# Kernel optimization log

Measured on AMD Instinct MI355X. Metric: run time of the kernel, lower is better.

## Reference

```python
import jax, jax.numpy as jnp
import numpy as np

B, S, W = 64, 512, 16
E, TE, CE, CC = 300, 50, 50, 50
HID, TGT = 256, 16
VOCAB, TAGV, CHARV = 5002, 50, 100
IN = E + TE + CC  # 400


def setup_inputs() -> dict:
    key = jax.random.key(0)
    ks = jax.random.split(key, 24)
    sc = 0.1
    embed_table = (jax.random.normal(ks[0], (VOCAB, E)) * sc).at[0].set(0.0)
    tag_table = (jax.random.normal(ks[1], (TAGV, TE)) * sc).at[0].set(0.0)
    char_table = (jax.random.normal(ks[2], (CHARV, CE)) * sc).at[0].set(0.0)
    return {
        "X": jax.random.randint(ks[3], (B, S), 0, VOCAB),
        "labels_m": jax.random.uniform(ks[4], (B, S)),
        "tags": jax.random.randint(ks[5], (B, S), 0, TAGV),
        "chars": jax.random.randint(ks[6], (B, S, W), 0, CHARV),
        "embed_table": embed_table,
        "tag_table": tag_table,
        "char_table": char_table,
        "conv_w": jax.random.normal(ks[7], (CC, CE, 3)) * sc,
        "conv_b": jax.random.normal(ks[8], (CC,)) * sc,
        "w_ih_f": jax.random.normal(ks[9], (4 * HID, IN)) * sc,
        "w_hh_f": jax.random.normal(ks[10], (4 * HID, HID)) * sc,
        "b_ih_f": jax.random.normal(ks[11], (4 * HID,)) * sc,
        "b_hh_f": jax.random.normal(ks[12], (4 * HID,)) * sc,
        "w_ih_b": jax.random.normal(ks[13], (4 * HID, IN)) * sc,
        "w_hh_b": jax.random.normal(ks[14], (4 * HID, HID)) * sc,
        "b_ih_b": jax.random.normal(ks[15], (4 * HID,)) * sc,
        "b_hh_b": jax.random.normal(ks[16], (4 * HID,)) * sc,
        "fc_w": jax.random.normal(ks[17], (TGT, 2 * HID)) * sc,
        "fc_b": jax.random.normal(ks[18], (TGT,)) * sc,
        "A": jax.random.normal(ks[19], (TGT, TGT)),
        "wd": jax.random.normal(ks[20], (2 * HID,)),
    }


def _lstm_dir(xs, w_ih, w_hh, b_ih, b_hh, reverse):
    # xs: [S, B, IN] ; PyTorch gate order i,f,g,o
    h0 = jnp.zeros((xs.shape[1], w_hh.shape[1]), xs.dtype)

    def step(carry, x):
        h, c = carry
        g = x @ w_ih.T + h @ w_hh.T + (b_ih + b_hh)
        i, f, gg, o = jnp.split(g, 4, axis=-1)
        c = jax.nn.sigmoid(f) * c + jax.nn.sigmoid(i) * jnp.tanh(gg)
        h = jax.nn.sigmoid(o) * jnp.tanh(c)
        return (h, c), h

    _, hs = jax.lax.scan(step, (h0, h0), xs, reverse=reverse)
    return hs


def _features(X, labels_m, tags, chars, embed_table, tag_table, char_table,
              conv_w, conv_b, w_ih_f, w_hh_f, b_ih_f, b_hh_f,
              w_ih_b, w_hh_b, b_ih_b, b_hh_b, fc_w, fc_b, wd):
    embed = embed_table[X]          # [B,S,E]
    tag_embed = tag_table[tags]     # [B,S,TE]
    ce = char_table[chars]          # [B,S,W,CE]
    ce = ce.transpose(0, 3, 1, 2).reshape(B, CE, S * W)  # [B,CE,S*W]
    conv = jax.lax.conv_general_dilated(
        ce, conv_w, window_strides=(1,), padding=((1, 1),),
        dimension_numbers=("NCH", "OIH", "NCH")) + conv_b[None, :, None]
    char_conv = conv.reshape(B, CC, S, W).max(axis=3).transpose(0, 2, 1)  # [B,S,CC]
    feat = jnp.concatenate([embed, tag_embed, char_conv], axis=2)  # [B,S,IN]
    xs = feat.transpose(1, 0, 2)  # [S,B,IN]
    hf = _lstm_dir(xs, w_ih_f, w_hh_f, b_ih_f, b_hh_f, reverse=False)
    hb = _lstm_dir(xs, w_ih_b, w_hh_b, b_ih_b, b_hh_b, reverse=True)
    H = jnp.concatenate([hf, hb], axis=-1).transpose(1, 0, 2)  # [B,S,2H]
    H = H + labels_m[:, :, None] * wd[None, None, :]
    return H @ fc_w.T + fc_b  # [B,S,TGT]


def _viterbi(P, A):
    Xs = P.transpose(1, 0, 2)  # [S,B,T]
    b_idx = jnp.arange(P.shape[0])

    def vstep(delta, x):
        scores = delta[:, :, None] + A[None] + x[:, None, :]  # [B,prev,cur]
        return scores.max(axis=1), (scores.max(axis=1), scores.argmax(axis=1))

    deltaL, (drest, psis) = jax.lax.scan(vstep, Xs[0], Xs[1:])
    deltas = jnp.concatenate([Xs[0][None], drest], axis=0)  # [S,B,T]
    psi_end = deltaL.argmax(axis=1)                          # [B]
    score0 = deltaL[b_idx, psi_end]

    def back(carry, inp):
        tag, sc = carry
        psi_t, delta_t = inp
        prev = psi_t[b_idx, tag]
        return (prev, sc + delta_t[b_idx, prev]), prev

    (_, score), prevs = jax.lax.scan(back, (psi_end, score0),
                                     (psis, deltas[:-1]), reverse=True)
    path = jnp.concatenate([prevs, psi_end[None]], axis=0).T  # [B,S]
    return path, score


def reference(X, labels_m, tags, chars, embed_table, tag_table, char_table,
              conv_w, conv_b, w_ih_f, w_hh_f, b_ih_f, b_hh_f,
              w_ih_b, w_hh_b, b_ih_b, b_hh_b, fc_w, fc_b, A, wd):
    P = _features(X, labels_m, tags, chars, embed_table, tag_table, char_table,
                  conv_w, conv_b, w_ih_f, w_hh_f, b_ih_f, b_hh_f,
                  w_ih_b, w_hh_b, b_ih_b, b_hh_b, fc_w, fc_b, wd)
    return _viterbi(P, A)
```

## Files before the change

kernel.cpp:

```cpp
#include <hip/hip_runtime.h>


#define DEV __device__ __forceinline__
typedef unsigned short u16;
typedef unsigned int   u32;
typedef unsigned char  u8;
typedef signed char    s8;
using short8  = __attribute__((ext_vector_type(8))) short;
using f32x4   = __attribute__((ext_vector_type(4))) float;
using int4v   = __attribute__((ext_vector_type(4))) int;

DEV float bf2f(u16 u){ union{u32 i; float f;} v; v.i = ((u32)u)<<16; return v.f; }
DEV u16 f2bf(float f){ u32 x = __float_as_uint(f); return (u16)((x + 0x7fffu + ((x>>16)&1u)) >> 16); }
DEV float sigf(float x){ return __builtin_amdgcn_rcpf(1.f + __expf(-x)); }
DEV float tanh_f(float x){ return 1.f - 2.f*__builtin_amdgcn_rcpf(__expf(2.f*x) + 1.f); }

typedef __attribute__((address_space(1))) const u32 GU;
typedef __attribute__((address_space(3))) u32 LU;
DEV void gld_lds16(const void* g, void* l){
  __builtin_amdgcn_global_load_lds((GU*)g, (LU*)l, 16, 0, 0);
}
DEV void bar_l(){
  __builtin_amdgcn_sched_barrier(0);
  asm volatile("s_waitcnt lgkmcnt(0)" ::: "memory");
  __builtin_amdgcn_s_barrier();
  __builtin_amdgcn_sched_barrier(0);
}

static const size_t OFF_GI   = 0;
static const size_t OFF_P    = 0;
static const size_t OFF_DL   = OFF_P  + (size_t)32768*16*4;
static const size_t OFF_PSI  = OFF_DL + (size_t)32768*16*4;
static const size_t OFF_B    = (size_t)134217728;
static const size_t OFF_WIH  = OFF_B    + (size_t)33554432;
static const size_t OFF_WQ   = OFF_WIH  + (size_t)1703936;
static const size_t OFF_SC   = OFF_WQ   + (size_t)524288;
static const size_t OFF_BIAS = OFF_SC   + 8192;
static const size_t OFF_WFC  = OFF_BIAS + 8192;
static const size_t REQUIRED = OFF_WFC  + 256;

__global__ void k0_pack(const float* __restrict__ wihf, const float* __restrict__ wihb,
                        u16* __restrict__ wih)
{
  int n = blockIdx.x, tid = threadIdx.x;
  const float* src = (n < 1024) ? (wihf + (size_t)n*400) : (wihb + (size_t)(n-1024)*400);
  u32* dst = (u32*)(wih + (size_t)n*416);
  if (tid < 208){
    int j = tid*2;
    u32 v = 0u;
    if (j < 400){
      float2 f = *(const float2*)(src + j);
      v = (u32)f2bf(f.x) | ((u32)f2bf(f.y) << 16);
    }
    dst[tid] = v;
  }
}

__global__ __launch_bounds__(256) void k0qm(
    const float* __restrict__ whhf, const float* __restrict__ whhb,
    s8* __restrict__ wq, float* __restrict__ sc2,
    const float* bihf, const float* bhhf, const float* bihb, const float* bhhb,
    const float* fcw, const float* wdp, float* bias, float* wfc)
{
  __shared__ float red[256];
  const int tid = threadIdx.x;
  if (blockIdx.x == 512){
    for (int n = tid; n < 2048; n += 256){
      bias[n] = (n < 1024) ? (bihf[n] + bhhf[n]) : (bihb[n-1024] + bhhb[n-1024]);
    }
    const int cur = tid & 15, part = tid >> 4;
    float s = 0.f;
    for (int k = part*32; k < part*32 + 32; k++) s += fcw[cur*512 + k] * wdp[k];
    red[tid] = s;
    __syncthreads();
    if (tid < 16){
      float t = 0.f;
      #pragma unroll
      for (int p = 0; p < 16; p++) t += red[p*16 + tid];
      wfc[tid] = t;
    }
    return;
  }
  const int row = blockIdx.x*4 + (tid >> 6);
  const int lane = tid & 63;
  const float* src = (row < 1024) ? (whhf + (size_t)row*256)
                                  : (whhb + (size_t)(row-1024)*256);
  f32x4 v = *(const f32x4*)(src + lane*4);
  float m = fmaxf(fmaxf(fabsf(v[0]), fabsf(v[1])), fmaxf(fabsf(v[2]), fabsf(v[3])));
  #pragma unroll
  for (int d = 1; d < 64; d <<= 1) m = fmaxf(m, __shfl_xor(m, d, 64));
  float inv = 127.f / (m + 1e-30f);
  u32 pack = 0;
  #pragma unroll
  for (int e = 0; e < 4; e++){
    int q = (int)rintf(v[e]*inv);
    q = q > 127 ? 127 : (q < -127 ? -127 : q);
    pack |= ((u32)(u8)(s8)q) << (8*e);
  }
  const int dir = row >> 10, n = row & 1023;
  const int g = n >> 8, j = n & 255, w2 = j >> 4, lr2 = j & 15;
  const int kk = lane >> 4, lq2 = (lane >> 2) & 3, e4 = lane & 3;
  u32* wq32 = (u32*)wq;
  wq32[dir*65536 + (((g*16 + w2)*4 + kk)*64 + lq2*16 + lr2)*4 + e4] = pack;
  if (lane == 0) sc2[row] = m * (1.f/16129.f);
}

__global__ __launch_bounds__(256) void k1_feat(
    const int* __restrict__ X, const int* __restrict__ tg, const int* __restrict__ ch,
    const float* __restrict__ etab, const float* __restrict__ ttab, const float* __restrict__ ctab,
    const float* __restrict__ cw, const float* __restrict__ cb, u16* __restrict__ feat)
{
  const int b = blockIdx.y, tid = threadIdx.x;
  __shared__ float ce_s[66*60];
  __shared__ float w_s[150*52];
  for (int i = tid; i < 7500; i += 256){
    int cc = i/150, r2 = i - cc*150;
    int ce = r2/3, dc = r2 - ce*3;
    w_s[(cc*3 + dc)*52 + ce] = cw[i];
  }
  const int li = tid & 15, jg = tid >> 4;

  for (int it = 0; it < 8; it++){
    const int sb = blockIdx.x*8 + it;
    __syncthreads();
    for (int i = tid; i < 600; i += 256){
      int wl = i/150, j = i - wl*150;
      int s = sb*4 + wl;
      int idx = X[b*512 + s];
      float2 f = *(const float2*)(etab + (size_t)idx*300 + j*2);
      *(u32*)(feat + (size_t)(s*64 + b)*416 + j*2) = (u32)f2bf(f.x) | ((u32)f2bf(f.y) << 16);
    }
    for (int i = tid; i < 100; i += 256){
      int wl = i/25, j = i - wl*25;
      int s = sb*4 + wl;
      int idx = tg[b*512 + s];
      float2 f = *(const float2*)(ttab + (size_t)idx*50 + j*2);
      *(u32*)(feat + (size_t)(s*64 + b)*416 + 300 + j*2) = (u32)f2bf(f.x) | ((u32)f2bf(f.y) << 16);
    }
    if (tid < 32){
      int wl = tid>>3, j = tid&7;
      int s = sb*4 + wl;
      *(u32*)(feat + (size_t)(s*64 + b)*416 + 400 + j*2) = 0u;
    }
    for (int i = tid; i < 3300; i += 256){
      int qq = i/50, ce = i - qq*50;
      int p = sb*64 - 1 + qq;
      float v = 0.f;
      if (p >= 0 && p < 8192){
        int ci = ch[b*8192 + p];
        v = ctab[ci*50 + ce];
      }
      ce_s[qq*60 + ce] = v;
    }
    __syncthreads();
    float acc[4][3];
    #pragma unroll
    for (int k=0;k<4;k++){ acc[k][0]=0.f; acc[k][1]=0.f; acc[k][2]=0.f; }
    #pragma unroll
    for (int dc = 0; dc < 3; dc++){
      for (int ceb = 0; ceb < 48; ceb += 4){
        f32x4 w0 = *(const f32x4*)&w_s[((3*jg+0)*3 + dc)*52 + ceb];
        f32x4 w1 = *(const f32x4*)&w_s[((3*jg+1)*3 + dc)*52 + ceb];
        f32x4 w2 = *(const f32x4*)&w_s[((3*jg+2)*3 + dc)*52 + ceb];
        #pragma unroll
        for (int k = 0; k < 4; k++){
          f32x4 cv = *(const f32x4*)&ce_s[(16*k + li + dc)*60 + ceb];
          #pragma unroll
          for (int e = 0; e < 4; e++){
            acc[k][0] += cv[e]*w0[e];
            acc[k][1] += cv[e]*w1[e];
            acc[k][2] += cv[e]*w2[e];
          }
        }
      }
      float w0a = w_s[((3*jg+0)*3+dc)*52 + 48], w0b = w_s[((3*jg+0)*3+dc)*52 + 49];
      float w1a = w_s[((3*jg+1)*3+dc)*52 + 48], w1b = w_s[((3*jg+1)*3+dc)*52 + 49];
      float w2a = w_s[((3*jg+2)*3+dc)*52 + 48], w2b = w_s[((3*jg+2)*3+dc)*52 + 49];
      #pragma unroll
      for (int k = 0; k < 4; k++){
        float ca = ce_s[(16*k + li + dc)*60 + 48];
        float cb2 = ce_s[(16*k + li + dc)*60 + 49];
        acc[k][0] += ca*w0a + cb2*w0b;
        acc[k][1] += ca*w1a + cb2*w1b;
        acc[k][2] += ca*w2a + cb2*w2b;
      }
    }
    #pragma unroll
    for (int m = 1; m < 16; m <<= 1)
      #pragma unroll
      for (int k=0;k<4;k++)
        #pragma unroll
        for (int c=0;c<3;c++)
          acc[k][c] = fmaxf(acc[k][c], __shfl_xor(acc[k][c], m, 64));
    if (li == 0){
      #pragma unroll
      for (int k=0;k<4;k++)
        #pragma unroll
        for (int c=0;c<3;c++){
          int cc = 3*jg + c;
          int s = sb*4 + k;
          feat[(size_t)(s*64 + b)*416 + 350 + cc] = f2bf(acc[k][c] + cb[cc]);
        }
    }
    if (tid < 128){
      int pl = tid & 63, cc = 48 + (tid >> 6);
      float a2 = 0.f;
      #pragma unroll
      for (int dc = 0; dc < 3; dc++){
        for (int ceb = 0; ceb < 48; ceb += 4){
          f32x4 wv = *(const f32x4*)&w_s[(cc*3 + dc)*52 + ceb];
          f32x4 cv = *(const f32x4*)&ce_s[(pl + dc)*60 + ceb];
          a2 += cv[0]*wv[0] + cv[1]*wv[1] + cv[2]*wv[2] + cv[3]*wv[3];
        }
        a2 += ce_s[(pl+dc)*60 + 48]*w_s[(cc*3+dc)*52 + 48]
            + ce_s[(pl+dc)*60 + 49]*w_s[(cc*3+dc)*52 + 49];
      }
      #pragma unroll
      for (int m = 1; m < 16; m <<= 1) a2 = fmaxf(a2, __shfl_xor(a2, m, 64));
      if ((tid & 15) == 0){
        int s = sb*4 + ((tid & 63) >> 4);
        feat[(size_t)(s*64 + b)*416 + 350 + cc] = f2bf(a2 + cb[cc]);
      }
    }
  }
}

__global__ __launch_bounds__(256) void k2_gemm(
    const u16* __restrict__ featp, const u16* __restrict__ wihp,
    const float* __restrict__ bias, u16* __restrict__ gi)
{
  const int m0 = blockIdx.y*128, n0 = blockIdx.x*128;
  const int tid = threadIdx.x, wv = tid>>6, lane = tid&63;
  const int lr = lane & 15, lq = lane >> 4;
  const int wm = (wv>>1)*64, wn = (wv&1)*64;
  __shared__ u16 As[4096], Bs[4096];
  f32x4 acc[4][4];
  #pragma unroll
  for (int a=0;a<4;a++)
    #pragma unroll
    for (int c=0;c<4;c++) acc[a][c] = (f32x4){0.f,0.f,0.f,0.f};
  for (int k0 = 0; k0 < 416; k0 += 32){
    __syncthreads();
    #pragma unroll
    for (int i = 0; i < 2; i++){
      int c = i*4 + wv;
      gld_lds16(featp + (size_t)(m0 + c*16 + (lane>>2))*416 + k0 + (lane&3)*8, &As[c*512]);
      gld_lds16(wihp  + (size_t)(n0 + c*16 + (lane>>2))*416 + k0 + (lane&3)*8, &Bs[c*512]);
    }
    __syncthreads();
    short8 af[4], bfr[4];
    #pragma unroll
    for (int mt=0; mt<4; mt++) af[mt]  = *(const short8*)(As + (wm + mt*16 + lr)*32 + lq*8);
    #pragma unroll
    for (int nt=0; nt<4; nt++) bfr[nt] = *(const short8*)(Bs + (wn + nt*16 + lr)*32 + lq*8);
    #pragma unroll
    for (int mt=0; mt<4; mt++)
      #pragma unroll
      for (int nt=0; nt<4; nt++)
        acc[mt][nt] = __builtin_amdgcn_mfma_f32_16x16x32_bf16(af[mt], bfr[nt], acc[mt][nt], 0,0,0);
  }
  #pragma unroll
  for (int nt=0; nt<4; nt++){
    float bv = bias[n0 + wn + nt*16 + lr];
    #pragma unroll
    for (int mt=0; mt<4; mt++)
      #pragma unroll
      for (int r=0; r<4; r++)
        gi[(size_t)(m0 + wm + mt*16 + lq*4 + r)*2048 + n0 + wn + nt*16 + lr]
            = f2bf(acc[mt][nt][r] + bv);
  }
}

__global__ __launch_bounds__(512, 2) void k3_lstm(
    const s8* __restrict__ wq, const float* __restrict__ sc2,
    const u16* __restrict__ gi, u16* __restrict__ hcat)
{
  const int dir = blockIdx.x >> 5;
  const int bb  = (blockIdx.x & 31) * 2;
  const int tid = threadIdx.x;
  const int w = tid >> 6, lane = tid & 63;
  const int lr = lane & 15, lq = lane >> 4;
  const int cb = tid >> 8, cj = tid & 255;

  __shared__ s8 Hs[2][4096];
  __shared__ float xbuf[2048];

  const s8* wqd = wq + dir*262144;
  int4v bq[2][4][4];
  #pragma unroll
  for (int sl = 0; sl < 2; sl++)
    #pragma unroll
    for (int g = 0; g < 4; g++)
      #pragma unroll
      for (int kk = 0; kk < 4; kk++)
        bq[sl][g][kk] = *(const int4v*)(wqd + (((((g*16 + 2*w + sl)*4 + kk)*64) + lane) << 4));

  float scl[4];
  #pragma unroll
  for (int g = 0; g < 4; g++) scl[g] = sc2[dir*1024 + g*256 + cj];

  *(uint2*)&Hs[0][tid*8] = (uint2){0u,0u};
  *(uint2*)&Hs[1][tid*8] = (uint2){0u,0u};

  float cst = 0.f;
  const ptrdiff_t dstep = dir ? -(ptrdiff_t)131072 : (ptrdiff_t)131072;
  const u16* g0 = gi + (size_t)((dir ? 511 : 0)*64 + bb + cb)*2048 + dir*1024 + cj;
  u32 gcur[4], gn1[4], gn2[4];
  #pragma unroll
  for (int g = 0; g < 4; g++) gcur[g] = g0[g*256];
  const u16* g1 = g0 + dstep;
  #pragma unroll
  for (int g = 0; g < 4; g++) gn1[g] = g1[g*256];
  const u16* gpref = g1;
  __syncthreads();

  #pragma unroll 1
  for (int t = 0; t < 512; t++){
    const int s = dir ? (511 - t) : t;
    if (t + 2 < 512) gpref += dstep;
    #pragma unroll
    for (int g = 0; g < 4; g++) gn2[g] = gpref[g*256];
    const s8* hb = Hs[t & 1];
    int4v aq[4];
    #pragma unroll
    for (int kk = 0; kk < 4; kk++)
      aq[kk] = *(const int4v*)(hb + lr*256 + ((kk*64 + lq*16) ^ (lr << 4)));
    int4v acc[2][4];
    #pragma unroll
    for (int sl = 0; sl < 2; sl++)
      #pragma unroll
      for (int g = 0; g < 4; g++) acc[sl][g] = (int4v){0,0,0,0};
    #pragma unroll
    for (int kk = 0; kk < 4; kk++)
      #pragma unroll
      for (int sl = 0; sl < 2; sl++)
        #pragma unroll
        for (int g = 0; g < 4; g++)
          acc[sl][g] = __builtin_amdgcn_mfma_i32_16x16x64_i8(aq[kk], bq[sl][g][kk], acc[sl][g], 0,0,0);
    if (lq == 0){
      #pragma unroll
      for (int sl = 0; sl < 2; sl++){
        const int j = (2*w + sl)*16 + lr;
        #pragma unroll
        for (int r = 0; r < 2; r++){
          f32x4 v = (f32x4){(float)acc[sl][0][r], (float)acc[sl][1][r],
                            (float)acc[sl][2][r], (float)acc[sl][3][r]};
          *(f32x4*)&xbuf[(r*256 + j)*4] = v;
        }
      }
    }
    bar_l();
    f32x4 p = *(const f32x4*)&xbuf[tid*4];
    float g4[4];
    #pragma unroll
    for (int g = 0; g < 4; g++) g4[g] = bf2f((u16)gcur[g]) + p[g]*scl[g];
    float iv = sigf(g4[0]), fv = sigf(g4[1]);
    float gg = tanh_f(g4[2]), ov = sigf(g4[3]);
    float c = fv*cst + iv*gg;
    cst = c;
    float h = ov * tanh_f(c);
    hcat[(size_t)(s*64 + bb + cb)*512 + dir*256 + cj] = f2bf(h);
    Hs[(t + 1) & 1][cb*256 + (cj ^ (cb << 4))] = (s8)(int)rintf(h * 127.f);
    #pragma unroll
    for (int g = 0; g < 4; g++){ gcur[g] = gn1[g]; gn1[g] = gn2[g]; }
    bar_l();
  }
}

__global__ __launch_bounds__(256) void k4_fc(
    const u16* __restrict__ hcat, const float* __restrict__ fcw, const float* __restrict__ fcb,
    const float* __restrict__ lmp, const float* __restrict__ wfc, float* __restrict__ Pout)
{
  const int wv = threadIdx.x >> 6, lane = threadIdx.x & 63;
  const int lr = lane & 15, lq = lane >> 4;
  const int mt = blockIdx.x*4 + wv;
  short8 bfr[16];
  #pragma unroll
  for (int kk = 0; kk < 16; kk++){
    const float* wr = fcw + (size_t)lr*512 + kk*32 + lq*8;
    f32x4 w0 = *(const f32x4*)wr;
    f32x4 w1 = *(const f32x4*)(wr + 4);
    short8 sv;
    #pragma unroll
    for (int e = 0; e < 4; e++){ sv[e] = (short)f2bf(w0[e]); sv[4+e] = (short)f2bf(w1[e]); }
    bfr[kk] = sv;
  }
  f32x4 acc = (f32x4){0.f,0.f,0.f,0.f};
  #pragma unroll
  for (int kk = 0; kk < 16; kk++){
    short8 af = *(const short8*)(hcat + (size_t)(mt*16 + lr)*512 + kk*32 + lq*8);
    acc = __builtin_amdgcn_mfma_f32_16x16x32_bf16(af, bfr[kk], acc, 0,0,0);
  }
  const int cur = lr;
  float fb = fcb[cur];
  float wf = wfc[cur];
  #pragma unroll
  for (int r = 0; r < 4; r++){
    int m = mt*16 + lq*4 + r;
    int b = m & 63, s = m >> 6;
    float lmv = lmp[b*512 + s];
    Pout[(size_t)m*16 + cur] = acc[r] + fb + lmv*wf;
  }
}

__global__ __launch_bounds__(64) void k5_vit(
    const float* __restrict__ Pg, const float* __restrict__ Am,
    float* __restrict__ dout, float* __restrict__ dl, u8* __restrict__ psi)
{
  const int b = blockIdx.x, lane = threadIdx.x;
  const int cur = lane >> 2, q = lane & 3;
  float Ar[4];
  #pragma unroll
  for (int r = 0; r < 4; r++) Ar[r] = Am[(4*q + r)*16 + cur];
  float val = Pg[(size_t)b*16 + cur];
  if (q == 0) dl[(size_t)b*16 + cur] = val;

#define FSTEP(X, S) { \
    float best = -3.0e38f; int bi = 0; \
    _Pragma("unroll") \
    for (int r = 0; r < 4; r++){ \
      float dp = __shfl(val, (4*q + r)*4, 64); \
      float sc = (dp + Ar[r]) + (X); \
      if (sc > best){ best = sc; bi = 4*q + r; } \
    } \
    { float ov = __shfl_xor(best, 1, 64); int oi = __shfl_xor(bi, 1, 64); \
      if (ov > best || (ov == best && oi < bi)){ best = ov; bi = oi; } } \
    { float ov = __shfl_xor(best, 2, 64); int oi = __shfl_xor(bi, 2, 64); \
      if (ov > best || (ov == best && oi < bi)){ best = ov; bi = oi; } } \
    val = best; \
    if (q == 0){ \
      dl[(size_t)((S)*64 + b)*16 + cur] = best; \
      psi[(size_t)((S)*64 + b)*16 + cur] = (u8)bi; \
    } }

  float x0 = Pg[(size_t)(1*64 + b)*16 + cur];
  float x1 = Pg[(size_t)(2*64 + b)*16 + cur];
  float x2 = Pg[(size_t)(3*64 + b)*16 + cur];
  float x3 = Pg[(size_t)(4*64 + b)*16 + cur];
  for (int s = 1; s < 512; s += 4){
    FSTEP(x0, s);
    if (s + 4 < 512) x0 = Pg[(size_t)((s+4)*64 + b)*16 + cur];
    if (s + 1 < 512) FSTEP(x1, s+1);
    if (s + 5 < 512) x1 = Pg[(size_t)((s+5)*64 + b)*16 + cur];
    if (s + 2 < 512) FSTEP(x2, s+2);
    if (s + 6 < 512) x2 = Pg[(size_t)((s+6)*64 + b)*16 + cur];
    if (s + 3 < 512) FSTEP(x3, s+3);
    if (s + 7 < 512) x3 = Pg[(size_t)((s+7)*64 + b)*16 + cur];
  }
#undef FSTEP

  float bv = val; int bix = cur;
  #pragma unroll
  for (int m = 1; m < 64; m <<= 1){
    float ov = __shfl_xor(bv, m, 64);
    int   oi = __shfl_xor(bix, m, 64);
    if (ov > bv || (ov == bv && oi < bix)){ bv = ov; bix = oi; }
  }
  int tag = bix;
  float score = bv;
  if (lane == 0) dout[b*512 + 511] = (float)tag;

#define BSTEP(PV, DV, T) { \
    int prev = __shfl((PV), tag, 64); \
    score += __shfl((DV), prev, 64); \
    if (lane == 0) dout[b*512 + (T)] = (float)prev; \
    tag = prev; }

  int   p0 = 0, p1 = 0, p2 = 0, p3 = 0;
  float d0 = 0.f, d1 = 0.f, d2 = 0.f, d3 = 0.f;
  if (lane < 16){
    p0 = psi[(size_t)(511*64 + b)*16 + lane]; d0 = dl[(size_t)(510*64 + b)*16 + lane];
    p1 = psi[(size_t)(510*64 + b)*16 + lane]; d1 = dl[(size_t)(509*64 + b)*16 + lane];
    p2 = psi[(size_t)(509*64 + b)*16 + lane]; d2 = dl[(size_t)(508*64 + b)*16 + lane];
    p3 = psi[(size_t)(508*64 + b)*16 + lane]; d3 = dl[(size_t)(507*64 + b)*16 + lane];
  }
  for (int t = 510; t >= 0; t -= 4){
    BSTEP(p0, d0, t);
    if (t - 4 >= 0 && lane < 16){
      p0 = psi[(size_t)((t-3)*64 + b)*16 + lane]; d0 = dl[(size_t)((t-4)*64 + b)*16 + lane];
    }
    if (t - 1 >= 0) BSTEP(p1, d1, t-1);
    if (t - 5 >= 0 && lane < 16){
      p1 = psi[(size_t)((t-4)*64 + b)*16 + lane]; d1 = dl[(size_t)((t-5)*64 + b)*16 + lane];
    }
    if (t - 2 >= 0) BSTEP(p2, d2, t-2);
    if (t - 6 >= 0 && lane < 16){
      p2 = psi[(size_t)((t-5)*64 + b)*16 + lane]; d2 = dl[(size_t)((t-6)*64 + b)*16 + lane];
    }
    if (t - 3 >= 0) BSTEP(p3, d3, t-3);
    if (t - 7 >= 0 && lane < 16){
      p3 = psi[(size_t)((t-6)*64 + b)*16 + lane]; d3 = dl[(size_t)((t-7)*64 + b)*16 + lane];
    }
  }
#undef BSTEP
  if (lane == 0) dout[32768 + b] = score;
}

extern "C" void kernel_launch(void* const* d_in, const int* in_sizes, int n_in,
                              void* d_out, int out_size, void* d_ws, size_t ws_size,
                              hipStream_t stream)
{
  (void)in_sizes; (void)n_in; (void)out_size;
  if (ws_size < REQUIRED) return;

  const int*   X    = (const int*)d_in[0];
  const float* lm   = (const float*)d_in[1];
  const int*   tg   = (const int*)d_in[2];
  const int*   ch   = (const int*)d_in[3];
  const float* etab = (const float*)d_in[4];
  const float* ttab = (const float*)d_in[5];
  const float* ctab = (const float*)d_in[6];
  const float* cw   = (const float*)d_in[7];
  const float* cb   = (const float*)d_in[8];
  const float* wihf = (const float*)d_in[9];
  const float* whhf = (const float*)d_in[10];
  const float* bihf = (const float*)d_in[11];
  const float* bhhf = (const float*)d_in[12];
  const float* wihb = (const float*)d_in[13];
  const float* whhb = (const float*)d_in[14];
  const float* bihb = (const float*)d_in[15];
  const float* bhhb = (const float*)d_in[16];
  const float* fcw  = (const float*)d_in[17];
  const float* fcb  = (const float*)d_in[18];
  const float* Am   = (const float*)d_in[19];
  const float* wdp  = (const float*)d_in[20];

  char* ws = (char*)d_ws;
  u16*   gi   = (u16*)(ws + OFF_GI);
  u16*   feat = (u16*)(ws + OFF_B);
  u16*   hcat = (u16*)(ws + OFF_B);
  u16*   wih  = (u16*)(ws + OFF_WIH);
  s8*    wq   = (s8*)(ws + OFF_WQ);
  float* sc2  = (float*)(ws + OFF_SC);
  float* Pg   = (float*)(ws + OFF_P);
  float* dlt  = (float*)(ws + OFF_DL);
  u8*    psi  = (u8*)(ws + OFF_PSI);
  float* bias = (float*)(ws + OFF_BIAS);
  float* wfc  = (float*)(ws + OFF_WFC);
  float* dout = (float*)d_out;

  k0_pack<<<2048, 256, 0, stream>>>(wihf, wihb, wih);
  k0qm<<<513, 256, 0, stream>>>(whhf, whhb, wq, sc2,
                                bihf, bhhf, bihb, bhhb, fcw, wdp, bias, wfc);
  k1_feat<<<dim3(16, 64), 256, 0, stream>>>(X, tg, ch, etab, ttab, ctab, cw, cb, feat);
  k2_gemm<<<dim3(16, 256), 256, 0, stream>>>(feat, wih, bias, gi);
  k3_lstm<<<64, 512, 0, stream>>>(wq, sc2, gi, hcat);
  k4_fc<<<512, 256, 0, stream>>>(hcat, fcw, fcb, lm, wfc, Pg);
  k5_vit<<<64, 64, 0, stream>>>(Pg, Am, dout, dlt, psi);
}
```

Before: 1.194 ms.

## Merge weight-prep kernels, raise MFMA priority, rework Viterbi with readlane broadcasts

Merges the two weight-preparation kernels into a single launch to save one kernel launch. Raises wave priority around the int8 MFMA block in the LSTM recurrence. Rewrites the Viterbi forward step so each lane computes a full 16-way max tree from scalar-broadcast deltas (readlane) instead of cross-lane shuffles, and uses readlane in backtracking. This trades shuffle latency on the serial critical path for more per-lane ALU work and scalar broadcasts. The argmax tie-break order in the tree may differ from the previous code.

```diff
diff --git a/kernel.cpp b/kernel.cpp
--- a/kernel.cpp
+++ b/kernel.cpp
@@ -14,6 +14,9 @@
 DEV u16 f2bf(float f){ u32 x = __float_as_uint(f); return (u16)((x + 0x7fffu + ((x>>16)&1u)) >> 16); }
 DEV float sigf(float x){ return __builtin_amdgcn_rcpf(1.f + __expf(-x)); }
 DEV float tanh_f(float x){ return 1.f - 2.f*__builtin_amdgcn_rcpf(__expf(2.f*x) + 1.f); }
+DEV float rdlane_f(float v, int l){
+  return __uint_as_float(__builtin_amdgcn_readlane(__float_as_uint(v), l));
+}
 
 typedef __attribute__((address_space(1))) const u32 GU;
 typedef __attribute__((address_space(3))) u32 LU;
@@ -39,32 +42,32 @@
 static const size_t OFF_WFC  = OFF_BIAS + 8192;
 static const size_t REQUIRED = OFF_WFC  + 256;
 
-__global__ void k0_pack(const float* __restrict__ wihf, const float* __restrict__ wihb,
-                        u16* __restrict__ wih)
-{
-  int n = blockIdx.x, tid = threadIdx.x;
-  const float* src = (n < 1024) ? (wihf + (size_t)n*400) : (wihb + (size_t)(n-1024)*400);
-  u32* dst = (u32*)(wih + (size_t)n*416);
-  if (tid < 208){
-    int j = tid*2;
-    u32 v = 0u;
-    if (j < 400){
-      float2 f = *(const float2*)(src + j);
-      v = (u32)f2bf(f.x) | ((u32)f2bf(f.y) << 16);
-    }
-    dst[tid] = v;
-  }
-}
-
-__global__ __launch_bounds__(256) void k0qm(
+__global__ __launch_bounds__(256) void k0_all(
     const float* __restrict__ whhf, const float* __restrict__ whhb,
     s8* __restrict__ wq, float* __restrict__ sc2,
     const float* bihf, const float* bhhf, const float* bihb, const float* bhhb,
-    const float* fcw, const float* wdp, float* bias, float* wfc)
+    const float* fcw, const float* wdp, float* bias, float* wfc,
+    const float* __restrict__ wihf, const float* __restrict__ wihb, u16* __restrict__ wih)
 {
   __shared__ float red[256];
   const int tid = threadIdx.x;
-  if (blockIdx.x == 512){
+  const int bx = blockIdx.x;
+  if (bx > 512){
+    const int n = bx - 513;
+    const float* src = (n < 1024) ? (wihf + (size_t)n*400) : (wihb + (size_t)(n-1024)*400);
+    u32* dst = (u32*)(wih + (size_t)n*416);
+    if (tid < 208){
+      int j = tid*2;
+      u32 v = 0u;
+      if (j < 400){
+        float2 f = *(const float2*)(src + j);
+        v = (u32)f2bf(f.x) | ((u32)f2bf(f.y) << 16);
+      }
+      dst[tid] = v;
+    }
+    return;
+  }
+  if (bx == 512){
     for (int n = tid; n < 2048; n += 256){
       bias[n] = (n < 1024) ? (bihf[n] + bhhf[n]) : (bihb[n-1024] + bhhb[n-1024]);
     }
@@ -81,7 +84,7 @@
     }
     return;
   }
-  const int row = blockIdx.x*4 + (tid >> 6);
+  const int row = bx*4 + (tid >> 6);
   const int lane = tid & 63;
   const float* src = (row < 1024) ? (whhf + (size_t)row*256)
                                   : (whhb + (size_t)(row-1024)*256);
@@ -330,6 +333,7 @@
     for (int sl = 0; sl < 2; sl++)
       #pragma unroll
       for (int g = 0; g < 4; g++) acc[sl][g] = (int4v){0,0,0,0};
+    __builtin_amdgcn_s_setprio(1);
     #pragma unroll
     for (int kk = 0; kk < 4; kk++)
       #pragma unroll
@@ -337,6 +341,7 @@
         #pragma unroll
         for (int g = 0; g < 4; g++)
           acc[sl][g] = __builtin_amdgcn_mfma_i32_16x16x64_i8(aq[kk], bq[sl][g][kk], acc[sl][g], 0,0,0);
+    __builtin_amdgcn_s_setprio(0);
     if (lq == 0){
       #pragma unroll
       for (int sl = 0; sl < 2; sl++){
@@ -408,30 +413,44 @@
     float* __restrict__ dout, float* __restrict__ dl, u8* __restrict__ psi)
 {
   const int b = blockIdx.x, lane = threadIdx.x;
-  const int cur = lane >> 2, q = lane & 3;
-  float Ar[4];
-  #pragma unroll
-  for (int r = 0; r < 4; r++) Ar[r] = Am[(4*q + r)*16 + cur];
-  float val = Pg[(size_t)b*16 + cur];
-  if (q == 0) dl[(size_t)b*16 + cur] = val;
+  const int cur = lane & 15;
+  float Ar[16];
+  #pragma unroll
+  for (int p = 0; p < 16; p++) Ar[p] = Am[p*16 + cur];
+  float dreg[16];
+  {
+    float v0 = Pg[(size_t)b*16 + cur];
+    if (lane < 16) dl[(size_t)b*16 + cur] = v0;
+    #pragma unroll
+    for (int c = 0; c < 16; c++) dreg[c] = rdlane_f(v0, c);
+  }
 
 #define FSTEP(X, S) { \
-    float best = -3.0e38f; int bi = 0; \
+    float v_[16]; \
     _Pragma("unroll") \
-    for (int r = 0; r < 4; r++){ \
-      float dp = __shfl(val, (4*q + r)*4, 64); \
-      float sc = (dp + Ar[r]) + (X); \
-      if (sc > best){ best = sc; bi = 4*q + r; } \
-    } \
-    { float ov = __shfl_xor(best, 1, 64); int oi = __shfl_xor(bi, 1, 64); \
-      if (ov > best || (ov == best && oi < bi)){ best = ov; bi = oi; } } \
-    { float ov = __shfl_xor(best, 2, 64); int oi = __shfl_xor(bi, 2, 64); \
-      if (ov > best || (ov == best && oi < bi)){ best = ov; bi = oi; } } \
-    val = best; \
-    if (q == 0){ \
+    for (int p = 0; p < 16; p++) v_[p] = dreg[p] + Ar[p]; \
+    float m1[8]; int i1[8]; \
+    _Pragma("unroll") \
+    for (int k = 0; k < 8; k++){ bool c_ = v_[2*k] >= v_[2*k+1]; \
+      m1[k] = c_ ? v_[2*k] : v_[2*k+1]; i1[k] = c_ ? 2*k : 2*k+1; } \
+    float m2[4]; int i2[4]; \
+    _Pragma("unroll") \
+    for (int k = 0; k < 4; k++){ bool c_ = m1[2*k] >= m1[2*k+1]; \
+      m2[k] = c_ ? m1[2*k] : m1[2*k+1]; i2[k] = c_ ? i1[2*k] : i1[2*k+1]; } \
+    float m3[2]; int i3[2]; \
+    _Pragma("unroll") \
+    for (int k = 0; k < 2; k++){ bool c_ = m2[2*k] >= m2[2*k+1]; \
+      m3[k] = c_ ? m2[2*k] : m2[2*k+1]; i3[k] = c_ ? i2[2*k] : i2[2*k+1]; } \
+    bool cf_ = m3[0] >= m3[1]; \
+    float best = (cf_ ? m3[0] : m3[1]) + (X); \
+    int bi = cf_ ? i3[0] : i3[1]; \
+    if (lane < 16){ \
       dl[(size_t)((S)*64 + b)*16 + cur] = best; \
       psi[(size_t)((S)*64 + b)*16 + cur] = (u8)bi; \
-    } }
+    } \
+    _Pragma("unroll") \
+    for (int c = 0; c < 16; c++) dreg[c] = rdlane_f(best, c); \
+  }
 
   float x0 = Pg[(size_t)(1*64 + b)*16 + cur];
   float x1 = Pg[(size_t)(2*64 + b)*16 + cur];
@@ -449,20 +468,16 @@
   }
 #undef FSTEP
 
-  float bv = val; int bix = cur;
-  #pragma unroll
-  for (int m = 1; m < 64; m <<= 1){
-    float ov = __shfl_xor(bv, m, 64);
-    int   oi = __shfl_xor(bix, m, 64);
-    if (ov > bv || (ov == bv && oi < bix)){ bv = ov; bix = oi; }
-  }
+  float bv = dreg[0]; int bix = 0;
+  #pragma unroll
+  for (int c = 1; c < 16; c++){ if (dreg[c] > bv){ bv = dreg[c]; bix = c; } }
   int tag = bix;
   float score = bv;
   if (lane == 0) dout[b*512 + 511] = (float)tag;
 
 #define BSTEP(PV, DV, T) { \
-    int prev = __shfl((PV), tag, 64); \
-    score += __shfl((DV), prev, 64); \
+    int prev = __builtin_amdgcn_readlane((PV), tag); \
+    score += rdlane_f((DV), prev); \
     if (lane == 0) dout[b*512 + (T)] = (float)prev; \
     tag = prev; }
 
@@ -539,9 +554,9 @@
   float* wfc  = (float*)(ws + OFF_WFC);
   float* dout = (float*)d_out;
 
-  k0_pack<<<2048, 256, 0, stream>>>(wihf, wihb, wih);
-  k0qm<<<513, 256, 0, stream>>>(whhf, whhb, wq, sc2,
-                                bihf, bhhf, bihb, bhhb, fcw, wdp, bias, wfc);
+  k0_all<<<2561, 256, 0, stream>>>(whhf, whhb, wq, sc2,
+                                   bihf, bhhf, bihb, bhhb, fcw, wdp, bias, wfc,
+                                   wihf, wihb, wih);
   k1_feat<<<dim3(16, 64), 256, 0, stream>>>(X, tg, ch, etab, ttab, ctab, cw, cb, feat);
   k2_gemm<<<dim3(16, 256), 256, 0, stream>>>(feat, wih, bias, gi);
   k3_lstm<<<64, 512, 0, stream>>>(wq, sc2, gi, hcat);
```

Measured after the change: 1.076 ms. 9.9% less time.
